# Performance work log

Measured on AMD Instinct MI355X. Metric: run time of the kernel, lower is better.

The kernel has to match this reference:

```python
import jax, jax.numpy as jnp
import numpy as np

B, Q, K, H, D = 4, 256, 256, 768, 768
NUM_LEN = 100  # length_embedding rows


def setup_inputs() -> dict:
    key = jax.random.key(0)
    ks = jax.random.split(key, 9)
    q = jax.random.normal(ks[0], (B, Q, H), jnp.float32)
    k = jax.random.normal(ks[1], (B, K, H), jnp.float32)
    m = jax.random.normal(ks[2], (B, K, D), jnp.float32)
    length_mask = jax.random.randint(ks[3], (B, Q, K), 0, NUM_LEN)
    attention_mask = jax.random.uniform(ks[4], (B, Q, K), jnp.float32)
    emb = jax.random.normal(ks[5], (NUM_LEN, H), jnp.float32) * 0.02
    # xavier-uniform-ish init for the two small Linears
    W1 = jax.random.normal(ks[6], (1, H), jnp.float32) * (1.0 / np.sqrt(H))
    b1 = jnp.zeros((1,), jnp.float32)
    W2 = jax.random.normal(ks[7], (5, H), jnp.float32) * (1.0 / np.sqrt(H))
    b2 = jnp.zeros((5,), jnp.float32)
    return {"q": q, "k": k, "m": m, "attention_mask": attention_mask,
            "emb": emb, "W1": W1, "b1": b1, "W2": W2, "b2": b2,
            "length_mask": length_mask}


def reference(q, k, m, attention_mask, emb, W1, b1, W2, b2, length_mask):
    # broadcast-add: q[B,Q,1,H] + k[B,1,K,H] + length_embedding[length_mask] -> [B,Q,K,H]
    s = q[:, :, None, :] + k[:, None, :, :] + emb[length_mask]
    # att_liner: H -> 1, squeezed -> [B,Q,K]
    attention_scores = jnp.einsum('bqkh,h->bqk', s, W1[0]) + b1[0]
    # att2_liner: H -> 5, softmax over the 5 classes -> [B,Q,K,5]
    scores = jax.nn.softmax(jnp.einsum('bqkh,ch->bqkc', s, W2) + b2, axis=-1)
    # multiplicative mask, then softmax over K
    attention_scores = attention_scores * attention_mask
    attention_probs = jax.nn.softmax(attention_scores, axis=-1)
    # dropout(p=0.2) is identity in eval mode
    attention_content = jnp.einsum('bqk,bkd->bqd', attention_probs, m)
    return attention_content, scores
```

## Files before the change

kernel.cpp:

```cpp
#include <hip/hip_runtime.h>


#define Hn 768
#define Bn 4
#define Qn 256
#define Kn 256
#define Dn 768

#define WS_KP 8192
#define WS_EP 16384
#define WS_PROBS 17408

__global__ __launch_bounds__(256) void proj_kernel(
    const float* __restrict__ q, const float* __restrict__ k,
    const float* __restrict__ emb, const float* __restrict__ W1,
    const float* __restrict__ W2, float* __restrict__ ws)
{
    int wid  = blockIdx.x * 4 + (threadIdx.x >> 6);
    int lane = threadIdx.x & 63;
    const float* src;
    float* dst;
    if (wid < 1024)      { src = q + wid * Hn;            dst = ws + wid * 8; }
    else if (wid < 2048) { src = k + (wid - 1024) * Hn;   dst = ws + WS_KP + (wid - 1024) * 8; }
    else {
        int r = wid - 2048;
        if (r >= 100) return;
        src = emb + r * Hn; dst = ws + WS_EP + r * 8;
    }
    float acc[6] = {0.f, 0.f, 0.f, 0.f, 0.f, 0.f};
    #pragma unroll
    for (int i = 0; i < 3; ++i) {
        int h = i * 256 + lane * 4;
        float4 x  = *(const float4*)&src[h];
        float4 w1 = *(const float4*)&W1[h];
        acc[0] += x.x * w1.x + x.y * w1.y + x.z * w1.z + x.w * w1.w;
        #pragma unroll
        for (int c = 0; c < 5; ++c) {
            float4 w2 = *(const float4*)&W2[c * Hn + h];
            acc[1 + c] += x.x * w2.x + x.y * w2.y + x.z * w2.z + x.w * w2.w;
        }
    }
    #pragma unroll
    for (int j = 0; j < 6; ++j) {
        float v = acc[j];
        #pragma unroll
        for (int off = 32; off > 0; off >>= 1)
            v += __shfl_xor(v, off, 64);
        if (lane == 0) dst[j] = v;
    }
}

__global__ __launch_bounds__(256) void score_kernel(
    const float* __restrict__ ws_proj, const float* __restrict__ am,
    const int* __restrict__ lm, const float* __restrict__ b1,
    const float* __restrict__ b2, float* __restrict__ scores_out,
    float* __restrict__ probs_out)
{
    const float* qP = ws_proj;
    const float* kP = ws_proj + WS_KP;
    const float* eP = ws_proj + WS_EP;
    int bq = blockIdx.x;
    int b  = bq >> 8;
    int t  = threadIdx.x;
    int wave = t >> 6, lane = t & 63;

    float qp[6];
    #pragma unroll
    for (int j = 0; j < 6; ++j) qp[j] = qP[bq * 8 + j];

    int krow = b * Kn + t;
    float4 ka = *(const float4*)&kP[krow * 8];
    float4 kb = *(const float4*)&kP[krow * 8 + 4];
    float kp[6] = {ka.x, ka.y, ka.z, ka.w, kb.x, kb.y};

    int l = lm[(size_t)bq * Kn + t];
    float4 ea = *(const float4*)&eP[l * 8];
    float4 eb = *(const float4*)&eP[l * 8 + 4];
    float ep[6] = {ea.x, ea.y, ea.z, ea.w, eb.x, eb.y};

    float amv = am[(size_t)bq * Kn + t];
    float as  = (qp[0] + kp[0] + ep[0] + b1[0]) * amv;

    __shared__ float sc[Kn * 5];
    float lg[5];
    float mx5 = -1e30f;
    #pragma unroll
    for (int c = 0; c < 5; ++c) {
        lg[c] = qp[c + 1] + kp[c + 1] + ep[c + 1] + b2[c];
        mx5 = fmaxf(mx5, lg[c]);
    }
    float s5 = 0.f;
    #pragma unroll
    for (int c = 0; c < 5; ++c) { lg[c] = __expf(lg[c] - mx5); s5 += lg[c]; }
    float inv5 = 1.f / s5;
    #pragma unroll
    for (int c = 0; c < 5; ++c) sc[t * 5 + c] = lg[c] * inv5;

    __shared__ float wmaxA[4], wsumA[4];
    float wm = as;
    #pragma unroll
    for (int off = 32; off > 0; off >>= 1) wm = fmaxf(wm, __shfl_xor(wm, off, 64));
    if (lane == 0) wmaxA[wave] = wm;
    __syncthreads();
    float mx = fmaxf(fmaxf(wmaxA[0], wmaxA[1]), fmaxf(wmaxA[2], wmaxA[3]));
    float e = __expf(as - mx);
    float wsum = e;
    #pragma unroll
    for (int off = 32; off > 0; off >>= 1) wsum += __shfl_xor(wsum, off, 64);
    if (lane == 0) wsumA[wave] = wsum;
    __syncthreads();
    float inv = 1.f / (wsumA[0] + wsumA[1] + wsumA[2] + wsumA[3]);
    probs_out[(size_t)bq * Kn + t] = e * inv;

    float4* so4 = (float4*)(scores_out + (size_t)bq * Kn * 5);
    const float4* sc4 = (const float4*)sc;
    so4[t] = sc4[t];
    if (t < 64) so4[256 + t] = sc4[256 + t];
}

__global__ __launch_bounds__(256) void pv_kernel(
    const float* __restrict__ probs, const float* __restrict__ m,
    float* __restrict__ out)
{
    int bid = blockIdx.x;
    int dt = bid % 6;
    int qt = (bid / 6) & 31;
    int b  = bid / 192;
    __shared__ float p[8][Kn];
    __shared__ float part[8][128];
    int t = threadIdx.x;
    int kh = t >> 7;
    int c  = t & 127;
    int d  = dt * 128 + c;

    const float* psrc = probs + ((size_t)(b * Qn + qt * 8) * Kn);
    #pragma unroll
    for (int i = 0; i < 8; ++i) p[i][t] = psrc[t + i * Kn];
    __syncthreads();

    float acc[8] = {0.f, 0.f, 0.f, 0.f, 0.f, 0.f, 0.f, 0.f};
    const float* mb = m + (size_t)b * Kn * Dn + d;
    int k0 = kh * 128;
    for (int k = k0; k < k0 + 128; k += 4) {
        float mv0 = mb[(size_t)(k + 0) * Dn];
        float mv1 = mb[(size_t)(k + 1) * Dn];
        float mv2 = mb[(size_t)(k + 2) * Dn];
        float mv3 = mb[(size_t)(k + 3) * Dn];
        #pragma unroll
        for (int qi = 0; qi < 8; ++qi) {
            float4 pv = *(const float4*)&p[qi][k];
            acc[qi] = fmaf(pv.x, mv0, acc[qi]);
            acc[qi] = fmaf(pv.y, mv1, acc[qi]);
            acc[qi] = fmaf(pv.z, mv2, acc[qi]);
            acc[qi] = fmaf(pv.w, mv3, acc[qi]);
        }
    }
    if (kh == 1) {
        #pragma unroll
        for (int qi = 0; qi < 8; ++qi) part[qi][c] = acc[qi];
    }
    __syncthreads();
    if (kh == 0) {
        float* ob = out + ((size_t)(b * Qn + qt * 8) * Dn) + d;
        #pragma unroll
        for (int qi = 0; qi < 8; ++qi) ob[qi * Dn] = acc[qi] + part[qi][c];
    }
}

extern "C" void kernel_launch(void* const* d_in, const int* in_sizes, int n_in,
                              void* d_out, int out_size, void* d_ws, size_t ws_size,
                              hipStream_t stream) {
    const float* q   = (const float*)d_in[0];
    const float* k   = (const float*)d_in[1];
    const float* m   = (const float*)d_in[2];
    const float* am  = (const float*)d_in[3];
    const float* emb = (const float*)d_in[4];
    const float* W1  = (const float*)d_in[5];
    const float* b1  = (const float*)d_in[6];
    const float* W2  = (const float*)d_in[7];
    const float* b2  = (const float*)d_in[8];
    const int*   lm  = (const int*)d_in[9];

    float* out         = (float*)d_out;
    float* out_content = out;
    float* out_scores  = out + Bn * Qn * Dn;

    float* ws    = (float*)d_ws;
    float* probs = ws + WS_PROBS;

    proj_kernel<<<537, 256, 0, stream>>>(q, k, emb, W1, W2, ws);
    score_kernel<<<Bn * Qn, 256, 0, stream>>>(ws, am, lm, b1, b2, out_scores, probs);
    pv_kernel<<<Bn * (Qn / 8) * 6, 256, 0, stream>>>(probs, m, out_content);
}
```

Before: 27.33 us.

## Fuse score softmax into PV kernel and vectorize PV with float4 K-split

Merges the score/softmax kernel into the PV kernel. Each block recomputes the attention softmax for its 8 query rows directly into shared memory, and only the dt==0 blocks write the 5-class scores. This drops one kernel launch and the global round trip of the probs tensor. The PV loop now loads float4 columns of m, splits K eight ways, and reduces the partial sums through shared memory. The cost is that the per-row softmax is computed redundantly across the 6 d-tiles, and each query row adds extra barriers.

```diff
diff --git a/kernel.cpp b/kernel.cpp
--- a/kernel.cpp
+++ b/kernel.cpp
@@ -1,15 +1,17 @@
 #include <hip/hip_runtime.h>
-
 
 #define Hn 768
 #define Bn 4
 #define Qn 256
 #define Kn 256
 #define Dn 768
-
 #define WS_KP 8192
 #define WS_EP 16384
-#define WS_PROBS 17408
+
+__device__ __forceinline__ void fma4(float4& a, float s, const float4& v) {
+    a.x = fmaf(s, v.x, a.x); a.y = fmaf(s, v.y, a.y);
+    a.z = fmaf(s, v.z, a.z); a.w = fmaf(s, v.w, a.w);
+}
 
 __global__ __launch_bounds__(256) void proj_kernel(
     const float* __restrict__ q, const float* __restrict__ k,
@@ -50,121 +52,123 @@
     }
 }
 
-__global__ __launch_bounds__(256) void score_kernel(
-    const float* __restrict__ ws_proj, const float* __restrict__ am,
-    const int* __restrict__ lm, const float* __restrict__ b1,
-    const float* __restrict__ b2, float* __restrict__ scores_out,
-    float* __restrict__ probs_out)
+__global__ __launch_bounds__(256, 3) void fused_kernel(
+    const float* __restrict__ ws_proj, const float* __restrict__ m,
+    const float* __restrict__ am, const int* __restrict__ lm,
+    const float* __restrict__ b1, const float* __restrict__ b2,
+    float* __restrict__ scores_out, float* __restrict__ content_out)
 {
+    __shared__ float p[8][Kn];
+    __shared__ float4 parts[8][8][32];
+    __shared__ float sc[Kn * 5];
+    __shared__ float wmaxA[4], wsumA[4];
+
+    int bid = blockIdx.x;
+    int dt = bid % 6;
+    int qt = (bid / 6) & 31;
+    int b  = bid / 192;
+    int q0 = qt * 8;
+    int t = threadIdx.x;
+    int wave = t >> 6, lane = t & 63;
+
     const float* qP = ws_proj;
     const float* kP = ws_proj + WS_KP;
     const float* eP = ws_proj + WS_EP;
-    int bq = blockIdx.x;
-    int b  = bq >> 8;
-    int t  = threadIdx.x;
-    int wave = t >> 6, lane = t & 63;
-
-    float qp[6];
-    #pragma unroll
-    for (int j = 0; j < 6; ++j) qp[j] = qP[bq * 8 + j];
 
     int krow = b * Kn + t;
     float4 ka = *(const float4*)&kP[krow * 8];
     float4 kb = *(const float4*)&kP[krow * 8 + 4];
     float kp[6] = {ka.x, ka.y, ka.z, ka.w, kb.x, kb.y};
+    float b1v = b1[0];
+    float b2v[5] = {b2[0], b2[1], b2[2], b2[3], b2[4]};
 
-    int l = lm[(size_t)bq * Kn + t];
-    float4 ea = *(const float4*)&eP[l * 8];
-    float4 eb = *(const float4*)&eP[l * 8 + 4];
-    float ep[6] = {ea.x, ea.y, ea.z, ea.w, eb.x, eb.y};
+    for (int qi = 0; qi < 8; ++qi) {
+        int bq = b * Qn + q0 + qi;
+        float qp[6];
+        #pragma unroll
+        for (int j = 0; j < 6; ++j) qp[j] = qP[bq * 8 + j];
 
-    float amv = am[(size_t)bq * Kn + t];
-    float as  = (qp[0] + kp[0] + ep[0] + b1[0]) * amv;
+        int l = lm[(size_t)bq * Kn + t];
+        float4 ea = *(const float4*)&eP[l * 8];
+        float4 eb = *(const float4*)&eP[l * 8 + 4];
+        float ep[6] = {ea.x, ea.y, ea.z, ea.w, eb.x, eb.y};
 
-    __shared__ float sc[Kn * 5];
-    float lg[5];
-    float mx5 = -1e30f;
+        float amv = am[(size_t)bq * Kn + t];
+        float as  = (qp[0] + kp[0] + ep[0] + b1v) * amv;
+
+        float wm = as;
+        #pragma unroll
+        for (int off = 32; off > 0; off >>= 1) wm = fmaxf(wm, __shfl_xor(wm, off, 64));
+        if (lane == 0) wmaxA[wave] = wm;
+        __syncthreads();
+        float mx = fmaxf(fmaxf(wmaxA[0], wmaxA[1]), fmaxf(wmaxA[2], wmaxA[3]));
+        float e = __expf(as - mx);
+        float wsum = e;
+        #pragma unroll
+        for (int off = 32; off > 0; off >>= 1) wsum += __shfl_xor(wsum, off, 64);
+        if (lane == 0) wsumA[wave] = wsum;
+        __syncthreads();
+        float inv = 1.f / (wsumA[0] + wsumA[1] + wsumA[2] + wsumA[3]);
+        p[qi][t] = e * inv;
+
+        if (dt == 0) {
+            float lg[5];
+            float mx5 = -1e30f;
+            #pragma unroll
+            for (int c = 0; c < 5; ++c) {
+                lg[c] = qp[c + 1] + kp[c + 1] + ep[c + 1] + b2v[c];
+                mx5 = fmaxf(mx5, lg[c]);
+            }
+            float s5 = 0.f;
+            #pragma unroll
+            for (int c = 0; c < 5; ++c) { lg[c] = __expf(lg[c] - mx5); s5 += lg[c]; }
+            float inv5 = 1.f / s5;
+            #pragma unroll
+            for (int c = 0; c < 5; ++c) sc[t * 5 + c] = lg[c] * inv5;
+            __syncthreads();
+            float4* so4 = (float4*)(scores_out + (size_t)bq * Kn * 5);
+            const float4* sc4 = (const float4*)sc;
+            so4[t] = sc4[t];
+            if (t < 64) so4[256 + t] = sc4[256 + t];
+        }
+        __syncthreads();
+    }
+
+    int kh = t >> 5;
+    int c4 = t & 31;
+    float4 acc[8];
     #pragma unroll
-    for (int c = 0; c < 5; ++c) {
-        lg[c] = qp[c + 1] + kp[c + 1] + ep[c + 1] + b2[c];
-        mx5 = fmaxf(mx5, lg[c]);
+    for (int qi = 0; qi < 8; ++qi) acc[qi] = make_float4(0.f, 0.f, 0.f, 0.f);
+
+    #pragma unroll
+    for (int g = 0; g < 8; ++g) {
+        int k0 = (kh << 5) + (g << 2);
+        const float* mb = m + (size_t)(b * Kn + k0) * Dn + dt * 128 + (c4 << 2);
+        float4 m0 = *(const float4*)(mb);
+        float4 m1 = *(const float4*)(mb + Dn);
+        float4 m2 = *(const float4*)(mb + 2 * Dn);
+        float4 m3 = *(const float4*)(mb + 3 * Dn);
+        #pragma unroll
+        for (int qi = 0; qi < 8; ++qi) {
+            float4 pv = *(const float4*)&p[qi][k0];
+            fma4(acc[qi], pv.x, m0);
+            fma4(acc[qi], pv.y, m1);
+            fma4(acc[qi], pv.z, m2);
+            fma4(acc[qi], pv.w, m3);
+        }
     }
-    float s5 = 0.f;
     #pragma unroll
-    for (int c = 0; c < 5; ++c) { lg[c] = __expf(lg[c] - mx5); s5 += lg[c]; }
-    float inv5 = 1.f / s5;
-    #pragma unroll
-    for (int c = 0; c < 5; ++c) sc[t * 5 + c] = lg[c] * inv5;
-
-    __shared__ float wmaxA[4], wsumA[4];
-    float wm = as;
-    #pragma unroll
-    for (int off = 32; off > 0; off >>= 1) wm = fmaxf(wm, __shfl_xor(wm, off, 64));
-    if (lane == 0) wmaxA[wave] = wm;
-    __syncthreads();
-    float mx = fmaxf(fmaxf(wmaxA[0], wmaxA[1]), fmaxf(wmaxA[2], wmaxA[3]));
-    float e = __expf(as - mx);
-    float wsum = e;
-    #pragma unroll
-    for (int off = 32; off > 0; off >>= 1) wsum += __shfl_xor(wsum, off, 64);
-    if (lane == 0) wsumA[wave] = wsum;
-    __syncthreads();
-    float inv = 1.f / (wsumA[0] + wsumA[1] + wsumA[2] + wsumA[3]);
-    probs_out[(size_t)bq * Kn + t] = e * inv;
-
-    float4* so4 = (float4*)(scores_out + (size_t)bq * Kn * 5);
-    const float4* sc4 = (const float4*)sc;
-    so4[t] = sc4[t];
-    if (t < 64) so4[256 + t] = sc4[256 + t];
-}
-
-__global__ __launch_bounds__(256) void pv_kernel(
-    const float* __restrict__ probs, const float* __restrict__ m,
-    float* __restrict__ out)
-{
-    int bid = blockIdx.x;
-    int dt = bid % 6;
-    int qt = (bid / 6) & 31;
-    int b  = bid / 192;
-    __shared__ float p[8][Kn];
-    __shared__ float part[8][128];
-    int t = threadIdx.x;
-    int kh = t >> 7;
-    int c  = t & 127;
-    int d  = dt * 128 + c;
-
-    const float* psrc = probs + ((size_t)(b * Qn + qt * 8) * Kn);
-    #pragma unroll
-    for (int i = 0; i < 8; ++i) p[i][t] = psrc[t + i * Kn];
+    for (int qi = 0; qi < 8; ++qi) parts[kh][qi][c4] = acc[qi];
     __syncthreads();
 
-    float acc[8] = {0.f, 0.f, 0.f, 0.f, 0.f, 0.f, 0.f, 0.f};
-    const float* mb = m + (size_t)b * Kn * Dn + d;
-    int k0 = kh * 128;
-    for (int k = k0; k < k0 + 128; k += 4) {
-        float mv0 = mb[(size_t)(k + 0) * Dn];
-        float mv1 = mb[(size_t)(k + 1) * Dn];
-        float mv2 = mb[(size_t)(k + 2) * Dn];
-        float mv3 = mb[(size_t)(k + 3) * Dn];
-        #pragma unroll
-        for (int qi = 0; qi < 8; ++qi) {
-            float4 pv = *(const float4*)&p[qi][k];
-            acc[qi] = fmaf(pv.x, mv0, acc[qi]);
-            acc[qi] = fmaf(pv.y, mv1, acc[qi]);
-            acc[qi] = fmaf(pv.z, mv2, acc[qi]);
-            acc[qi] = fmaf(pv.w, mv3, acc[qi]);
-        }
+    int qi2 = t >> 5, c42 = t & 31;
+    float4 s = parts[0][qi2][c42];
+    #pragma unroll
+    for (int kk = 1; kk < 8; ++kk) {
+        float4 v = parts[kk][qi2][c42];
+        s.x += v.x; s.y += v.y; s.z += v.z; s.w += v.w;
     }
-    if (kh == 1) {
-        #pragma unroll
-        for (int qi = 0; qi < 8; ++qi) part[qi][c] = acc[qi];
-    }
-    __syncthreads();
-    if (kh == 0) {
-        float* ob = out + ((size_t)(b * Qn + qt * 8) * Dn) + d;
-        #pragma unroll
-        for (int qi = 0; qi < 8; ++qi) ob[qi * Dn] = acc[qi] + part[qi][c];
-    }
+    *(float4*)(content_out + (size_t)(b * Qn + q0 + qi2) * Dn + dt * 128 + (c42 << 2)) = s;
 }
 
 extern "C" void kernel_launch(void* const* d_in, const int* in_sizes, int n_in,
@@ -185,10 +189,9 @@
     float* out_content = out;
     float* out_scores  = out + Bn * Qn * Dn;
 
-    float* ws    = (float*)d_ws;
-    float* probs = ws + WS_PROBS;
+    float* ws = (float*)d_ws;
 
     proj_kernel<<<537, 256, 0, stream>>>(q, k, emb, W1, W2, ws);
-    score_kernel<<<Bn * Qn, 256, 0, stream>>>(ws, am, lm, b1, b2, out_scores, probs);
-    pv_kernel<<<Bn * (Qn / 8) * 6, 256, 0, stream>>>(probs, m, out_content);
+    fused_kernel<<<Bn * (Qn / 8) * 6, 256, 0, stream>>>(
+        ws, m, am, lm, b1, b2, out_scores, out_content);
 }
```

Result: slower. 30.44 us (+11.4%).
